# Kernel tuning notes

Hardware: AMD Instinct MI355X
Metric: run time of the kernel (lower is better)

The kernel has to match this reference:

```python
import jax, jax.numpy as jnp
import numpy as np

N_NODES = 8192
ADJ_LEN = 4096  # first half of codebook = adjective nodes, rest = noun nodes
E_DIM = 256
TOPK = 4
BETA = 0.25


def setup_inputs() -> dict:
    key = jax.random.key(0)
    ks = jax.random.split(key, 6)
    z = jax.random.normal(ks[0], (64, 2 * E_DIM, 16, 16), dtype=jnp.float32)
    node_x = jax.random.normal(ks[1], (N_NODES, 1024), dtype=jnp.float32)
    edge_index = jax.random.randint(ks[2], (2, 131072), 0, N_NODES, dtype=jnp.int32)
    W1 = jax.random.normal(ks[3], (1024, E_DIM), dtype=jnp.float32) * 0.02
    b1 = jnp.zeros((E_DIM,), dtype=jnp.float32)
    W2 = jax.random.normal(ks[4], (E_DIM, E_DIM), dtype=jnp.float32) * 0.02
    b2 = jnp.zeros((E_DIM,), dtype=jnp.float32)
    return {"z": z, "node_x": node_x, "edge_index": edge_index,
            "W1": W1, "b1": b1, "W2": W2, "b2": b2}


def gcn_conv(x, edge_index, W, b):
    # GCNConv: symmetric-normalized adjacency with self-loops, then linear.
    n = x.shape[0]
    loop = jnp.arange(n, dtype=edge_index.dtype)
    src = jnp.concatenate([edge_index[0], loop])
    dst = jnp.concatenate([edge_index[1], loop])
    xw = x @ W  # [n, out]
    deg = jax.ops.segment_sum(jnp.ones_like(dst, dtype=xw.dtype), dst, num_segments=n)
    dinv = jax.lax.rsqrt(jnp.maximum(deg, 1e-12))
    norm = dinv[src] * dinv[dst]  # [E+n]
    out = jax.ops.segment_sum(norm[:, None] * xw[src], dst, num_segments=n)
    return out + b


def pairwise_sqdist(zf, emb):
    # ||z||^2 + ||e||^2 - 2 z.e  -> [M, K]
    return (jnp.sum(zf * zf, axis=1, keepdims=True)
            + jnp.sum(emb * emb, axis=1)
            - 2.0 * zf @ emb.T)


def reference(z, node_x, edge_index, W1, b1, W2, b2):
    sg = jax.lax.stop_gradient
    # GCN over codebook graph (eval mode: dropout is identity)
    h = jax.nn.relu(gcn_conv(node_x, edge_index, W1, b1))
    tew = gcn_conv(h, edge_index, W2, b2)  # [N_NODES, E_DIM]

    b, c2, H, W = z.shape
    # ---- adjective branch: top-k gather + mean ----
    z_adj = jnp.transpose(z[:, :E_DIM], (0, 2, 3, 1))  # b h w c
    zf = z_adj.reshape(-1, E_DIM)  # [M, e_dim]
    emb_a = tew[:ADJ_LEN]
    d = pairwise_sqdist(zf, emb_a)
    _, idx1 = jax.lax.top_k(-d, TOPK)  # [M, topk] smallest distances
    z_adj_q = emb_a[idx1].mean(axis=1).reshape(z_adj.shape)

    quan_loss = jnp.mean((sg(z_adj_q) - z_adj) ** 2)
    commit_loss = BETA * jnp.mean((z_adj_q - sg(z_adj)) ** 2)
    loss = quan_loss + commit_loss
    z_adj_q = z_adj + sg(z_adj_q - z_adj)  # straight-through
    z_adj_q = jnp.transpose(z_adj_q, (0, 3, 1, 2))
    ind1 = idx1.reshape(b, H * W * TOPK)  # sane_index_shape, c=256

    # ---- noun branch: argmin ----
    z_noun = jnp.transpose(z[:, E_DIM:], (0, 2, 3, 1))
    zf = z_noun.reshape(-1, E_DIM)
    emb_n = tew[ADJ_LEN:]
    d = pairwise_sqdist(zf, emb_n)
    idx2 = jnp.argmin(d, axis=1)  # [M]
    z_noun_q = emb_n[idx2].reshape(z_noun.shape)

    q2 = jnp.mean((sg(z_noun_q) - z_noun) ** 2)
    c2_ = BETA * jnp.mean((z_noun_q - sg(z_noun)) ** 2)
    loss = loss + q2 + c2_
    commit_loss = commit_loss + c2_
    quan_loss = quan_loss + q2
    z_noun_q = z_noun + sg(z_noun_q - z_noun)
    z_noun_q = jnp.transpose(z_noun_q, (0, 3, 1, 2))
    ind2 = idx2.reshape(b, H * W)

    z_q = jnp.concatenate([z_adj_q, z_noun_q], axis=1)
    indices = jnp.concatenate([ind1, ind2], axis=1)
    return z_q, loss, commit_loss, quan_loss, indices
```

## Files before the change

### kernel.cpp

```cpp
#include <hip/hip_runtime.h>

#define N_NODES 8192
#define N_EDGES 131072
#define E_DIM 256
#define NE_HALF 4096
#define LOSS_OFF 8388608
#define IDX_OFF 8388611
#define KC_PANEL 384

#define WS_DINV 0
#define WS_EN2 8192
#define WS_LOSS 16384
#define WS_CNT 17408
#define WS_ROWSTART 25600
#define WS_FILL 34816
#define WS_COL 43008
#define WS_XW 174080
#define WS_H  2271232
#define WS_TEW 4368384
#define WS_QN2 6465536

__global__ void count_kernel(const int* __restrict__ dst, int* __restrict__ cnt) {
    int e = blockIdx.x * blockDim.x + threadIdx.x;
    if (e < N_EDGES) atomicAdd(&cnt[dst[e]], 1);
}

__global__ __launch_bounds__(1024) void scan_kernel(const int* __restrict__ cnt,
                                                    int* __restrict__ rowstart,
                                                    float* __restrict__ dinv) {
    __shared__ int part[1024];
    int t = threadIdx.x;
    int c[8], pre[8];
    int run = 0;
#pragma unroll
    for (int i = 0; i < 8; ++i) {
        c[i] = cnt[t * 8 + i];
        pre[i] = run;
        run += c[i];
    }
    part[t] = run;
    __syncthreads();
    for (int d = 1; d < 1024; d <<= 1) {
        int add = (t >= d) ? part[t - d] : 0;
        __syncthreads();
        part[t] += add;
        __syncthreads();
    }
    int off = (t == 0) ? 0 : part[t - 1];
#pragma unroll
    for (int i = 0; i < 8; ++i) {
        rowstart[t * 8 + i] = off + pre[i];
        dinv[t * 8 + i] = 1.0f / sqrtf((float)(c[i] + 1));
    }
    if (t == 1023) rowstart[8192] = part[1023];
}

__global__ void scatter_kernel(const int* __restrict__ dst,
                               const int* __restrict__ rowstart, int* __restrict__ fill,
                               int* __restrict__ col) {
    int e = blockIdx.x * blockDim.x + threadIdx.x;
    if (e < N_EDGES) {
        int d = dst[e];
        int pos = atomicAdd(&fill[d], 1);
        col[rowstart[d] + pos] = e;
    }
}

__global__ __launch_bounds__(256) void sort_kernel(const int* __restrict__ src,
                                                   const int* __restrict__ rowstart,
                                                   int* __restrict__ col) {
    int i = blockIdx.x * blockDim.x + threadIdx.x;
    if (i >= N_NODES) return;
    int s0 = rowstart[i], s1 = rowstart[i + 1];
    for (int a = s0 + 1; a < s1; ++a) {
        int v = col[a];
        int b = a - 1;
        while (b >= s0 && col[b] > v) { col[b + 1] = col[b]; --b; }
        col[b + 1] = v;
    }
    for (int a = s0; a < s1; ++a) col[a] = src[col[a]];
}

__global__ __launch_bounds__(256) void gemm_kernel(const float* __restrict__ X,
                                                   const float* __restrict__ W,
                                                   float* __restrict__ Y, int K) {
    __shared__ float aT[16][68];
    __shared__ float bT[16][68];
    const int t = threadIdx.x;
    const int bm = blockIdx.x * 64;
    const int bn = blockIdx.y * 64;
    float cacc[4][4] = {};
    const int tm = t >> 4, tn = t & 15;
    const int lm = t >> 2, lk = (t & 3) * 4;
    const int bk = t >> 4, bn4 = (t & 15) * 4;
    int kp = 0;
    bool first = true;
    while (kp < K) {
        int rem = K - kp;
        int pl;
        if (rem >= 2 * KC_PANEL) pl = KC_PANEL;
        else if (rem > KC_PANEL) pl = (rem / 2 + 15) & ~15;
        else pl = rem;
        const int kend = kp + pl;
        float pacc[4][4] = {};
        for (int k0 = kp; k0 < kend; k0 += 16) {
            __syncthreads();
            float4 av = *(const float4*)&X[(size_t)(bm + lm) * K + k0 + lk];
            aT[lk + 0][lm] = av.x; aT[lk + 1][lm] = av.y;
            aT[lk + 2][lm] = av.z; aT[lk + 3][lm] = av.w;
            *(float4*)&bT[bk][bn4] = *(const float4*)&W[(size_t)(k0 + bk) * E_DIM + bn + bn4];
            __syncthreads();
#pragma unroll
            for (int k = 0; k < 16; ++k) {
                float4 a = *(const float4*)&aT[k][tm * 4];
                float4 b = *(const float4*)&bT[k][tn * 4];
                float qa[4] = {a.x, a.y, a.z, a.w};
                float ea[4] = {b.x, b.y, b.z, b.w};
#pragma unroll
                for (int i = 0; i < 4; ++i)
#pragma unroll
                    for (int j = 0; j < 4; ++j) pacc[i][j] = fmaf(qa[i], ea[j], pacc[i][j]);
            }
        }
        if (first) {
#pragma unroll
            for (int i = 0; i < 4; ++i)
#pragma unroll
                for (int j = 0; j < 4; ++j) cacc[i][j] = pacc[i][j];
        } else {
#pragma unroll
            for (int i = 0; i < 4; ++i)
#pragma unroll
                for (int j = 0; j < 4; ++j) cacc[i][j] = __fadd_rn(cacc[i][j], pacc[i][j]);
        }
        first = false;
        kp = kend;
    }
#pragma unroll
    for (int i = 0; i < 4; ++i) {
        float4 v = make_float4(cacc[i][0], cacc[i][1], cacc[i][2], cacc[i][3]);
        *(float4*)&Y[(size_t)(bm + tm * 4 + i) * E_DIM + bn + tn * 4] = v;
    }
}

__global__ __launch_bounds__(256) void agg_kernel(const float* __restrict__ xw,
                                                  const int* __restrict__ rowstart,
                                                  const int* __restrict__ col,
                                                  const float* __restrict__ dinv,
                                                  const float* __restrict__ bias,
                                                  float* __restrict__ out, int do_relu) {
    int i = blockIdx.x;
    int c = threadIdx.x;
    float di = dinv[i];
    float acc = 0.0f;
    int s0 = rowstart[i], s1 = rowstart[i + 1];
    for (int j = s0; j < s1; ++j) {
        int s = col[j];
        float nrm = __fmul_rn(dinv[s], di);
        acc = __fadd_rn(acc, __fmul_rn(nrm, xw[(size_t)s * E_DIM + c]));
    }
    acc = __fadd_rn(acc, __fmul_rn(__fmul_rn(di, di), xw[(size_t)i * E_DIM + c]));
    acc = __fadd_rn(acc, bias[c]);
    if (do_relu) acc = fmaxf(acc, 0.0f);
    out[(size_t)i * E_DIM + c] = acc;
}

__global__ __launch_bounds__(256) void enorm_kernel(const float* __restrict__ e,
                                                    float* __restrict__ out) {
    int t = threadIdx.x;
    int row = blockIdx.x * 16 + (t >> 4);
    int l = t & 15;
    int blk = l >> 3, j = l & 7;
    const float* p = e + (size_t)row * 256 + blk * 128 + j;
    float v = p[0];
    float acc = __fmul_rn(v, v);
#pragma unroll
    for (int i = 1; i < 16; ++i) {
        float w = p[i * 8];
        acc = __fadd_rn(acc, __fmul_rn(w, w));
    }
    acc = __fadd_rn(acc, __shfl_xor(acc, 1, 64));
    acc = __fadd_rn(acc, __shfl_xor(acc, 2, 64));
    acc = __fadd_rn(acc, __shfl_xor(acc, 4, 64));
    acc = __fadd_rn(acc, __shfl_xor(acc, 8, 64));
    if (l == 0) out[row] = acc;
}

__global__ __launch_bounds__(256) void qnorm_kernel(const float* __restrict__ z,
                                                    float* __restrict__ out) {
    int t = threadIdx.x;
    int row = blockIdx.x * 16 + (t >> 4);
    int half = row >> 14, r = row & 16383;
    int b = r >> 8, pp = r & 255;
    int l = t & 15;
    int blk = l >> 3, j = l & 7;
    const float* p = z + (size_t)b * 131072 + (size_t)half * 65536 + pp +
                     (size_t)(blk * 128 + j) * 256;
    float v = p[0];
    float acc = __fmul_rn(v, v);
#pragma unroll
    for (int i = 1; i < 16; ++i) {
        float w = p[(size_t)i * 8 * 256];
        acc = __fadd_rn(acc, __fmul_rn(w, w));
    }
    acc = __fadd_rn(acc, __shfl_xor(acc, 1, 64));
    acc = __fadd_rn(acc, __shfl_xor(acc, 2, 64));
    acc = __fadd_rn(acc, __shfl_xor(acc, 4, 64));
    acc = __fadd_rn(acc, __shfl_xor(acc, 8, 64));
    if (l == 0) out[row] = acc;
}

__device__ __forceinline__ unsigned long long shfl_xor_u64(unsigned long long v, int m) {
    unsigned int lo = (unsigned int)v, hi = (unsigned int)(v >> 32);
    lo = __shfl_xor(lo, m, 64);
    hi = __shfl_xor(hi, m, 64);
    return ((unsigned long long)hi << 32) | lo;
}

template <int TK, int QM>
__device__ __forceinline__ void quant_body(const float* __restrict__ z,
                                           const float* __restrict__ emb,
                                           const float* __restrict__ en2,
                                           const float* __restrict__ qn2,
                                           unsigned long long* __restrict__ topWs,
                                           int coff) {
    constexpr int EP = QM / 2;
    constexpr int QB = 8 * QM;
    constexpr int EPB = NE_HALF / EP;
    constexpr int NET = EPB / 256;
    constexpr int QPAD = QB + 8;

    __shared__ float eT[32][264];
    __shared__ float qS[32][QPAD];
    __shared__ float sEn2[256];

    const int t = threadIdx.x;
    const int qt = blockIdx.x / EP;
    const int ep = blockIdx.x % EP;
    const int r0 = qt * QB;
    const int b = r0 >> 8;
    const int p0 = r0 & 255;
    const int e00 = ep * EPB;

    const int tq = t >> 5, te = t & 31;
    const int q0 = tq * QM;
    const int e0 = te * 4;

    const int sk = (t & 7) * 4;
    const int se = t >> 3;
    const int cb = se ^ (sk & 24);
    const int kq = t >> 3, jq = (t & 7) * 4;

    const float* zb = z + (size_t)b * 131072 + (size_t)coff * 256 + p0;

    float aq[QM];
#pragma unroll
    for (int i = 0; i < QM; ++i) aq[i] = qn2[r0 + q0 + i];

    unsigned long long bk[QM][TK];
#pragma unroll
    for (int i = 0; i < QM; ++i)
#pragma unroll
        for (int j = 0; j < TK; ++j) bk[i][j] = 0xFFFFFFFFFFFFFFFFull;

    for (int et = 0; et < NET; ++et) {
        const int ebase = e00 + et * 256;
        float acc[QM][8] = {};
        for (int kc = 0; kc < 8; ++kc) {
            __syncthreads();
#pragma unroll
            for (int i = 0; i < 8; ++i) {
                float4 v = *(const float4*)&emb[(size_t)(ebase + se + 32 * i) * 256 + kc * 32 + sk];
                eT[sk + 0][cb + 32 * i] = v.x;
                eT[sk + 1][cb + 32 * i] = v.y;
                eT[sk + 2][cb + 32 * i] = v.z;
                eT[sk + 3][cb + 32 * i] = v.w;
            }
            {
                float4 v = *(const float4*)&zb[(size_t)(kc * 32 + kq) * 256 + jq];
                *(float4*)&qS[kq][jq] = v;
                if (QM == 8) {
                    float4 w = *(const float4*)&zb[(size_t)(kc * 32 + kq) * 256 + jq + 32];
                    *(float4*)&qS[kq][jq + 32] = w;
                }
            }
            if (kc == 0) sEn2[t] = en2[ebase + t];
            __syncthreads();
#pragma unroll
            for (int k = 0; k < 32; ++k) {
                const int f = k & 24;
                const int c1 = e0 ^ f;
                float4 ea = *(const float4*)&eT[k][c1];
                float4 eb = *(const float4*)&eT[k][128 + c1];
                float ev[8] = {ea.x, ea.y, ea.z, ea.w, eb.x, eb.y, eb.z, eb.w};
                float qv[QM];
                {
                    float4 qa = *(const float4*)&qS[k][q0];
                    qv[0] = qa.x; qv[1] = qa.y; qv[2] = qa.z; qv[3] = qa.w;
                    if (QM == 8) {
                        float4 qb2 = *(const float4*)&qS[k][q0 + 4];
                        qv[4] = qb2.x; qv[5] = qb2.y; qv[6] = qb2.z; qv[7] = qb2.w;
                    }
                }
#pragma unroll
                for (int i = 0; i < QM; ++i)
#pragma unroll
                    for (int j = 0; j < 8; ++j)
                        acc[i][j] = fmaf(qv[i], ev[j], acc[i][j]);
            }
        }
#pragma unroll
        for (int j = 0; j < 8; ++j) {
            const int le = (j < 4) ? (e0 + j) : (128 + e0 + j - 4);
            float e2 = sEn2[le];
            unsigned int gi = (unsigned int)(ebase + le);
#pragma unroll
            for (int i = 0; i < QM; ++i) {
                float t1 = __fadd_rn(aq[i], e2);
                float s = __fsub_rn(t1, __fmul_rn(2.0f, acc[i][j]));
                unsigned long long key =
                    ((unsigned long long)__float_as_uint(s) << 32) | gi;
                if (key < bk[i][TK - 1]) {
                    bk[i][TK - 1] = key;
#pragma unroll
                    for (int mm = TK - 1; mm > 0; --mm)
                        if (bk[i][mm] < bk[i][mm - 1]) {
                            unsigned long long tmp = bk[i][mm];
                            bk[i][mm] = bk[i][mm - 1];
                            bk[i][mm - 1] = tmp;
                        }
                }
            }
        }
    }

#pragma unroll
    for (int mw = 1; mw < 32; mw <<= 1) {
#pragma unroll
        for (int i = 0; i < QM; ++i) {
            unsigned long long ms[TK], os[TK], ns[TK];
#pragma unroll
            for (int j = 0; j < TK; ++j) {
                ms[j] = bk[i][j];
                os[j] = shfl_xor_u64(bk[i][j], mw);
            }
#pragma unroll
            for (int x = 0; x < TK; ++x) {
                bool ta = ms[0] < os[0];
                ns[x] = ta ? ms[0] : os[0];
#pragma unroll
                for (int y = 0; y < TK - 1; ++y) {
                    ms[y] = ta ? ms[y + 1] : ms[y];
                    os[y] = ta ? os[y] : os[y + 1];
                }
            }
#pragma unroll
            for (int j = 0; j < TK; ++j) bk[i][j] = ns[j];
        }
    }

    if (te == 0) {
#pragma unroll
        for (int i = 0; i < QM; ++i) {
            unsigned long long* dst = topWs + ((size_t)(r0 + q0 + i) * EP + ep) * TK;
#pragma unroll
            for (int j = 0; j < TK; ++j) dst[j] = bk[i][j];
        }
    }
}

__global__ __launch_bounds__(256, 4) void quantA_kernel(const float* __restrict__ z,
                                                        const float* __restrict__ emb,
                                                        const float* __restrict__ en2,
                                                        const float* __restrict__ qn2,
                                                        unsigned long long* __restrict__ topWs) {
    quant_body<4, 4>(z, emb, en2, qn2, topWs, 0);
}

__global__ __launch_bounds__(256, 3) void quantN_kernel(const float* __restrict__ z,
                                                        const float* __restrict__ emb,
                                                        const float* __restrict__ en2,
                                                        const float* __restrict__ qn2,
                                                        unsigned long long* __restrict__ topWs) {
    quant_body<1, 8>(z, emb, en2, qn2, topWs, 256);
}

__global__ __launch_bounds__(256) void mergeA_kernel(const unsigned long long* __restrict__ topWs,
                                                     const float* __restrict__ z,
                                                     const float* __restrict__ emb,
                                                     float* __restrict__ out,
                                                     float* __restrict__ lossAcc) {
    __shared__ int sIdx[32][4];
    __shared__ float red[256];
    const int t = threadIdx.x;
    const int r0 = blockIdx.x * 32;
    const int b = r0 >> 8, p0 = r0 & 255;
    if (t < 32) {
        const unsigned long long* src = topWs + (size_t)(r0 + t) * 8;
        unsigned long long ms[4], os[4], ns[4];
#pragma unroll
        for (int j = 0; j < 4; ++j) { ms[j] = src[j]; os[j] = src[4 + j]; }
#pragma unroll
        for (int x = 0; x < 4; ++x) {
            bool ta = ms[0] < os[0];
            ns[x] = ta ? ms[0] : os[0];
#pragma unroll
            for (int y = 0; y < 3; ++y) {
                ms[y] = ta ? ms[y + 1] : ms[y];
                os[y] = ta ? os[y] : os[y + 1];
            }
        }
        int pp = p0 + t;
#pragma unroll
        for (int j = 0; j < 4; ++j) {
            int idx = (int)(unsigned int)(ns[j] & 0xffffffffull);
            sIdx[t][j] = idx;
            out[IDX_OFF + (size_t)b * 1280 + pp * 4 + j] = (float)idx;
        }
    }
    __syncthreads();
    float lsum = 0.0f;
    {
        const int q = t & 31;
        const int pp = p0 + q;
        float* ob = out + (size_t)b * 131072 + pp;
        const float* zb = z + (size_t)b * 131072 + pp;
        int id[4];
#pragma unroll
        for (int j = 0; j < 4; ++j) id[j] = sIdx[q][j];
        for (int i = 0; i < 32; ++i) {
            int c = (t >> 5) + 8 * i;
            float v = 0.0f;
#pragma unroll
            for (int j = 0; j < 4; ++j) v = __fadd_rn(v, emb[(size_t)id[j] * 256 + c]);
            v *= 0.25f;
            float dd = v - zb[(size_t)c * 256];
            lsum += dd * dd;
            ob[(size_t)c * 256] = v;
        }
    }
    red[t] = lsum;
    __syncthreads();
    for (int s2 = 128; s2 > 0; s2 >>= 1) {
        if (t < s2) red[t] += red[t + s2];
        __syncthreads();
    }
    if (t == 0) atomicAdd(lossAcc, red[0]);
}

__global__ __launch_bounds__(256) void mergeN_kernel(const unsigned long long* __restrict__ topWs,
                                                     const float* __restrict__ z,
                                                     const float* __restrict__ emb,
                                                     float* __restrict__ out,
                                                     float* __restrict__ lossAcc) {
    __shared__ int sIdx[32];
    __shared__ float red[256];
    const int t = threadIdx.x;
    const int r0 = blockIdx.x * 32;
    const int b = r0 >> 8, p0 = r0 & 255;
    if (t < 32) {
        const unsigned long long* src = topWs + (size_t)(r0 + t) * 4;
        unsigned long long k0 = src[0], k1 = src[1], k2 = src[2], k3 = src[3];
        unsigned long long m0 = (k0 < k1) ? k0 : k1;
        unsigned long long m1 = (k2 < k3) ? k2 : k3;
        unsigned long long mm = (m0 < m1) ? m0 : m1;
        int idx = (int)(unsigned int)(mm & 0xffffffffull);
        sIdx[t] = idx;
        out[IDX_OFF + (size_t)b * 1280 + 1024 + p0 + t] = (float)idx;
    }
    __syncthreads();
    float lsum = 0.0f;
    {
        const int q = t & 31;
        const int pp = p0 + q;
        float* ob = out + (size_t)b * 131072 + 65536 + pp;
        const float* zb = z + (size_t)b * 131072 + 65536 + pp;
        int id = sIdx[q];
        for (int i = 0; i < 32; ++i) {
            int c = (t >> 5) + 8 * i;
            float v = emb[(size_t)id * 256 + c];
            float dd = v - zb[(size_t)c * 256];
            lsum += dd * dd;
            ob[(size_t)c * 256] = v;
        }
    }
    red[t] = lsum;
    __syncthreads();
    for (int s2 = 128; s2 > 0; s2 >>= 1) {
        if (t < s2) red[t] += red[t + s2];
        __syncthreads();
    }
    if (t == 0) atomicAdd(lossAcc, red[0]);
}

__global__ void final_kernel(const float* __restrict__ lossAcc, float* __restrict__ out) {
    if (threadIdx.x == 0 && blockIdx.x == 0) {
        const float inv = 1.0f / 4194304.0f;
        float mseA = lossAcc[0] * inv;
        float mseN = lossAcc[1] * inv;
        float quan = mseA + mseN;
        float commit = 0.25f * mseA + 0.25f * mseN;
        out[LOSS_OFF + 0] = quan + commit;
        out[LOSS_OFF + 1] = commit;
        out[LOSS_OFF + 2] = quan;
    }
}

extern "C" void kernel_launch(void* const* d_in, const int* in_sizes, int n_in,
                              void* d_out, int out_size, void* d_ws, size_t ws_size,
                              hipStream_t stream) {
    const float* z = (const float*)d_in[0];
    const float* node_x = (const float*)d_in[1];
    const int* ei = (const int*)d_in[2];
    const float* W1 = (const float*)d_in[3];
    const float* b1 = (const float*)d_in[4];
    const float* W2 = (const float*)d_in[5];
    const float* b2 = (const float*)d_in[6];
    float* out = (float*)d_out;
    float* ws = (float*)d_ws;

    float* dinv = ws + WS_DINV;
    float* en2 = ws + WS_EN2;
    float* lossAcc = ws + WS_LOSS;
    int* cnt = (int*)(ws + WS_CNT);
    int* rowstart = (int*)(ws + WS_ROWSTART);
    int* fill = (int*)(ws + WS_FILL);
    int* col = (int*)(ws + WS_COL);
    float* xw = ws + WS_XW;
    float* h = ws + WS_H;
    float* tew = ws + WS_TEW;
    float* qn2 = ws + WS_QN2;
    unsigned long long* topA = (unsigned long long*)(ws + WS_XW);
    unsigned long long* topN = topA + 131072;

    const int* srcp = ei;
    const int* dstp = ei + N_EDGES;

    hipMemsetAsync(cnt, 0, N_NODES * sizeof(int), stream);
    hipMemsetAsync(fill, 0, N_NODES * sizeof(int), stream);
    hipMemsetAsync(lossAcc, 0, 2 * sizeof(float), stream);

    count_kernel<<<N_EDGES / 256, 256, 0, stream>>>(dstp, cnt);
    scan_kernel<<<1, 1024, 0, stream>>>(cnt, rowstart, dinv);
    scatter_kernel<<<N_EDGES / 256, 256, 0, stream>>>(dstp, rowstart, fill, col);
    sort_kernel<<<N_NODES / 256, 256, 0, stream>>>(srcp, rowstart, col);

    qnorm_kernel<<<2048, 256, 0, stream>>>(z, qn2);

    gemm_kernel<<<dim3(128, 4), 256, 0, stream>>>(node_x, W1, xw, 1024);
    agg_kernel<<<N_NODES, 256, 0, stream>>>(xw, rowstart, col, dinv, b1, h, 1);
    gemm_kernel<<<dim3(128, 4), 256, 0, stream>>>(h, W2, xw, 256);
    agg_kernel<<<N_NODES, 256, 0, stream>>>(xw, rowstart, col, dinv, b2, tew, 0);

    enorm_kernel<<<512, 256, 0, stream>>>(tew, en2);

    quantA_kernel<<<1024, 256, 0, stream>>>(z, tew, en2, qn2, topA);
    quantN_kernel<<<1024, 256, 0, stream>>>(z, tew + (size_t)NE_HALF * E_DIM,
                                            en2 + NE_HALF, qn2 + 16384, topN);
    mergeA_kernel<<<512, 256, 0, stream>>>(topA, z, tew, out, lossAcc + 0);
    mergeN_kernel<<<512, 256, 0, stream>>>(topN, z, tew + (size_t)NE_HALF * E_DIM,
                                           out, lossAcc + 1);
    final_kernel<<<1, 64, 0, stream>>>(lossAcc, out);
}
```

Measured before the change: 1.820 ms.

## Shrink quantizer register tile to 4x4 and track top-k as float/index pairs

The distance GEMM tile drops to 4 queries by 4 codebook entries per thread, over 128-entry codebook tiles. The codebook is now always split in two halves per query tile, so the noun merge reads 2 partial results instead of 4. The packed 64-bit keys in the running top-k and the wave shuffles are replaced by separate float score and int index registers, which avoids 64-bit compares and double shuffles. The smaller tile cuts register and LDS pressure and drops the occupancy hints, at the cost of fewer FMAs per LDS load and more tile-loop iterations.

```diff
diff --git a/kernel.cpp b/kernel.cpp
--- a/kernel.cpp
+++ b/kernel.cpp
@@ -210,40 +210,27 @@
     if (l == 0) out[row] = acc;
 }
 
-__device__ __forceinline__ unsigned long long shfl_xor_u64(unsigned long long v, int m) {
-    unsigned int lo = (unsigned int)v, hi = (unsigned int)(v >> 32);
-    lo = __shfl_xor(lo, m, 64);
-    hi = __shfl_xor(hi, m, 64);
-    return ((unsigned long long)hi << 32) | lo;
-}
-
-template <int TK, int QM>
+template <int TK>
 __device__ __forceinline__ void quant_body(const float* __restrict__ z,
                                            const float* __restrict__ emb,
                                            const float* __restrict__ en2,
                                            const float* __restrict__ qn2,
                                            unsigned long long* __restrict__ topWs,
                                            int coff) {
-    constexpr int EP = QM / 2;
-    constexpr int QB = 8 * QM;
-    constexpr int EPB = NE_HALF / EP;
-    constexpr int NET = EPB / 256;
-    constexpr int QPAD = QB + 8;
-
-    __shared__ float eT[32][264];
-    __shared__ float qS[32][QPAD];
-    __shared__ float sEn2[256];
+    __shared__ float eT[32][132];
+    __shared__ float qS[32][36];
+    __shared__ float sEn2[128];
 
     const int t = threadIdx.x;
-    const int qt = blockIdx.x / EP;
-    const int ep = blockIdx.x % EP;
-    const int r0 = qt * QB;
+    const int qt = blockIdx.x >> 1;
+    const int ep = blockIdx.x & 1;
+    const int r0 = qt * 32;
     const int b = r0 >> 8;
     const int p0 = r0 & 255;
-    const int e00 = ep * EPB;
+    const int e00 = ep * 2048;
 
     const int tq = t >> 5, te = t & 31;
-    const int q0 = tq * QM;
+    const int q0 = tq * 4;
     const int e0 = te * 4;
 
     const int sk = (t & 7) * 4;
@@ -253,83 +240,64 @@
 
     const float* zb = z + (size_t)b * 131072 + (size_t)coff * 256 + p0;
 
-    float aq[QM];
-#pragma unroll
-    for (int i = 0; i < QM; ++i) aq[i] = qn2[r0 + q0 + i];
-
-    unsigned long long bk[QM][TK];
-#pragma unroll
-    for (int i = 0; i < QM; ++i)
-#pragma unroll
-        for (int j = 0; j < TK; ++j) bk[i][j] = 0xFFFFFFFFFFFFFFFFull;
-
-    for (int et = 0; et < NET; ++et) {
-        const int ebase = e00 + et * 256;
-        float acc[QM][8] = {};
+    float aq[4];
+#pragma unroll
+    for (int i = 0; i < 4; ++i) aq[i] = qn2[r0 + q0 + i];
+
+    float bsr[4][TK];
+    int bir[4][TK];
+#pragma unroll
+    for (int i = 0; i < 4; ++i)
+#pragma unroll
+        for (int j = 0; j < TK; ++j) { bsr[i][j] = 3.4e38f; bir[i][j] = 0; }
+
+    for (int et = 0; et < 16; ++et) {
+        const int ebase = e00 + et * 128;
+        float acc[4][4] = {};
         for (int kc = 0; kc < 8; ++kc) {
             __syncthreads();
 #pragma unroll
-            for (int i = 0; i < 8; ++i) {
+            for (int i = 0; i < 4; ++i) {
                 float4 v = *(const float4*)&emb[(size_t)(ebase + se + 32 * i) * 256 + kc * 32 + sk];
                 eT[sk + 0][cb + 32 * i] = v.x;
                 eT[sk + 1][cb + 32 * i] = v.y;
                 eT[sk + 2][cb + 32 * i] = v.z;
                 eT[sk + 3][cb + 32 * i] = v.w;
             }
-            {
-                float4 v = *(const float4*)&zb[(size_t)(kc * 32 + kq) * 256 + jq];
-                *(float4*)&qS[kq][jq] = v;
-                if (QM == 8) {
-                    float4 w = *(const float4*)&zb[(size_t)(kc * 32 + kq) * 256 + jq + 32];
-                    *(float4*)&qS[kq][jq + 32] = w;
-                }
-            }
-            if (kc == 0) sEn2[t] = en2[ebase + t];
+            *(float4*)&qS[kq][jq] = *(const float4*)&zb[(size_t)(kc * 32 + kq) * 256 + jq];
+            if (kc == 0 && t < 128) sEn2[t] = en2[ebase + t];
             __syncthreads();
 #pragma unroll
             for (int k = 0; k < 32; ++k) {
                 const int f = k & 24;
-                const int c1 = e0 ^ f;
-                float4 ea = *(const float4*)&eT[k][c1];
-                float4 eb = *(const float4*)&eT[k][128 + c1];
-                float ev[8] = {ea.x, ea.y, ea.z, ea.w, eb.x, eb.y, eb.z, eb.w};
-                float qv[QM];
-                {
-                    float4 qa = *(const float4*)&qS[k][q0];
-                    qv[0] = qa.x; qv[1] = qa.y; qv[2] = qa.z; qv[3] = qa.w;
-                    if (QM == 8) {
-                        float4 qb2 = *(const float4*)&qS[k][q0 + 4];
-                        qv[4] = qb2.x; qv[5] = qb2.y; qv[6] = qb2.z; qv[7] = qb2.w;
+                float4 ev4 = *(const float4*)&eT[k][e0 ^ f];
+                float4 qv4 = *(const float4*)&qS[k][q0];
+                float qa[4] = {qv4.x, qv4.y, qv4.z, qv4.w};
+                float ea[4] = {ev4.x, ev4.y, ev4.z, ev4.w};
+#pragma unroll
+                for (int i = 0; i < 4; ++i)
+#pragma unroll
+                    for (int j = 0; j < 4; ++j) acc[i][j] = fmaf(qa[i], ea[j], acc[i][j]);
+            }
+        }
+#pragma unroll
+        for (int j = 0; j < 4; ++j) {
+            float e2 = sEn2[e0 + j];
+            int gi = ebase + e0 + j;
+#pragma unroll
+            for (int i = 0; i < 4; ++i) {
+                float t1 = __fadd_rn(aq[i], e2);
+                float s = __fsub_rn(t1, __fmul_rn(2.0f, acc[i][j]));
+                if (s < bsr[i][TK - 1]) {
+                    bsr[i][TK - 1] = s; bir[i][TK - 1] = gi;
+#pragma unroll
+                    for (int m = TK - 1; m > 0; --m) {
+                        if (bsr[i][m] < bsr[i][m - 1]) {
+                            float tf = bsr[i][m]; bsr[i][m] = bsr[i][m - 1]; bsr[i][m - 1] = tf;
+                            int ti2 = bir[i][m]; bir[i][m] = bir[i][m - 1]; bir[i][m - 1] = ti2;
+                        }
                     }
                 }
-#pragma unroll
-                for (int i = 0; i < QM; ++i)
-#pragma unroll
-                    for (int j = 0; j < 8; ++j)
-                        acc[i][j] = fmaf(qv[i], ev[j], acc[i][j]);
-            }
-        }
-#pragma unroll
-        for (int j = 0; j < 8; ++j) {
-            const int le = (j < 4) ? (e0 + j) : (128 + e0 + j - 4);
-            float e2 = sEn2[le];
-            unsigned int gi = (unsigned int)(ebase + le);
-#pragma unroll
-            for (int i = 0; i < QM; ++i) {
-                float t1 = __fadd_rn(aq[i], e2);
-                float s = __fsub_rn(t1, __fmul_rn(2.0f, acc[i][j]));
-                unsigned long long key =
-                    ((unsigned long long)__float_as_uint(s) << 32) | gi;
-                if (key < bk[i][TK - 1]) {
-                    bk[i][TK - 1] = key;
-#pragma unroll
-                    for (int mm = TK - 1; mm > 0; --mm)
-                        if (bk[i][mm] < bk[i][mm - 1]) {
-                            unsigned long long tmp = bk[i][mm];
-                            bk[i][mm] = bk[i][mm - 1];
-                            bk[i][mm - 1] = tmp;
-                        }
-                }
             }
         }
     }
@@ -337,52 +305,59 @@
 #pragma unroll
     for (int mw = 1; mw < 32; mw <<= 1) {
 #pragma unroll
-        for (int i = 0; i < QM; ++i) {
-            unsigned long long ms[TK], os[TK], ns[TK];
+        for (int i = 0; i < 4; ++i) {
+            float ms[TK], os[TK], ns[TK];
+            int mi[TK], oi[TK], ni[TK];
 #pragma unroll
             for (int j = 0; j < TK; ++j) {
-                ms[j] = bk[i][j];
-                os[j] = shfl_xor_u64(bk[i][j], mw);
+                ms[j] = bsr[i][j]; mi[j] = bir[i][j];
+                os[j] = __shfl_xor(bsr[i][j], mw, 64);
+                oi[j] = __shfl_xor(bir[i][j], mw, 64);
             }
 #pragma unroll
             for (int x = 0; x < TK; ++x) {
-                bool ta = ms[0] < os[0];
+                bool ta = (ms[0] < os[0]) || (ms[0] == os[0] && mi[0] < oi[0]);
                 ns[x] = ta ? ms[0] : os[0];
+                ni[x] = ta ? mi[0] : oi[0];
 #pragma unroll
                 for (int y = 0; y < TK - 1; ++y) {
                     ms[y] = ta ? ms[y + 1] : ms[y];
+                    mi[y] = ta ? mi[y + 1] : mi[y];
                     os[y] = ta ? os[y] : os[y + 1];
+                    oi[y] = ta ? oi[y] : oi[y + 1];
                 }
             }
 #pragma unroll
-            for (int j = 0; j < TK; ++j) bk[i][j] = ns[j];
+            for (int j = 0; j < TK; ++j) { bsr[i][j] = ns[j]; bir[i][j] = ni[j]; }
         }
     }
 
     if (te == 0) {
 #pragma unroll
-        for (int i = 0; i < QM; ++i) {
-            unsigned long long* dst = topWs + ((size_t)(r0 + q0 + i) * EP + ep) * TK;
-#pragma unroll
-            for (int j = 0; j < TK; ++j) dst[j] = bk[i][j];
-        }
-    }
-}
-
-__global__ __launch_bounds__(256, 4) void quantA_kernel(const float* __restrict__ z,
-                                                        const float* __restrict__ emb,
-                                                        const float* __restrict__ en2,
-                                                        const float* __restrict__ qn2,
-                                                        unsigned long long* __restrict__ topWs) {
-    quant_body<4, 4>(z, emb, en2, qn2, topWs, 0);
-}
-
-__global__ __launch_bounds__(256, 3) void quantN_kernel(const float* __restrict__ z,
-                                                        const float* __restrict__ emb,
-                                                        const float* __restrict__ en2,
-                                                        const float* __restrict__ qn2,
-                                                        unsigned long long* __restrict__ topWs) {
-    quant_body<1, 8>(z, emb, en2, qn2, topWs, 256);
+        for (int i = 0; i < 4; ++i) {
+            unsigned long long* dst = topWs + ((size_t)(r0 + q0 + i) * 2 + ep) * TK;
+#pragma unroll
+            for (int j = 0; j < TK; ++j)
+                dst[j] = ((unsigned long long)__float_as_uint(bsr[i][j]) << 32) |
+                         (unsigned int)bir[i][j];
+        }
+    }
+}
+
+__global__ __launch_bounds__(256) void quantA_kernel(const float* __restrict__ z,
+                                                     const float* __restrict__ emb,
+                                                     const float* __restrict__ en2,
+                                                     const float* __restrict__ qn2,
+                                                     unsigned long long* __restrict__ topWs) {
+    quant_body<4>(z, emb, en2, qn2, topWs, 0);
+}
+
+__global__ __launch_bounds__(256) void quantN_kernel(const float* __restrict__ z,
+                                                     const float* __restrict__ emb,
+                                                     const float* __restrict__ en2,
+                                                     const float* __restrict__ qn2,
+                                                     unsigned long long* __restrict__ topWs) {
+    quant_body<1>(z, emb, en2, qn2, topWs, 256);
 }
 
 __global__ __launch_bounds__(256) void mergeA_kernel(const unsigned long long* __restrict__ topWs,
@@ -459,11 +434,9 @@
     const int r0 = blockIdx.x * 32;
     const int b = r0 >> 8, p0 = r0 & 255;
     if (t < 32) {
-        const unsigned long long* src = topWs + (size_t)(r0 + t) * 4;
-        unsigned long long k0 = src[0], k1 = src[1], k2 = src[2], k3 = src[3];
-        unsigned long long m0 = (k0 < k1) ? k0 : k1;
-        unsigned long long m1 = (k2 < k3) ? k2 : k3;
-        unsigned long long mm = (m0 < m1) ? m0 : m1;
+        const unsigned long long* src = topWs + (size_t)(r0 + t) * 2;
+        unsigned long long k0 = src[0], k1 = src[1];
+        unsigned long long mm = (k0 < k1) ? k0 : k1;
         int idx = (int)(unsigned int)(mm & 0xffffffffull);
         sIdx[t] = idx;
         out[IDX_OFF + (size_t)b * 1280 + 1024 + p0 + t] = (float)idx;
```

Result: faster. 1.519 ms (-16.5%).
